# Kernel optimization log

Hardware: AMD Instinct MI355X
Metric: run time of the kernel (lower is better)

The kernel has to match this reference:

```python
import math
import jax, jax.numpy as jnp
import numpy as np

DIM = 1024
QK_DIM = 200
HIDDEN = 2 * DIM  # expansion_factor = 2
N = 8192


def setup_inputs() -> dict:
    key = jax.random.key(0)
    ks = jax.random.split(key, 8)
    s = 0.02
    return {
        "x": jax.random.normal(ks[0], (N, DIM), dtype=jnp.float32),
        "W_hidden": jax.random.normal(ks[1], (DIM, 2 * HIDDEN), dtype=jnp.float32) * s,
        "b_hidden": jnp.zeros((2 * HIDDEN,), dtype=jnp.float32),
        "W_qk": jax.random.normal(ks[2], (DIM, QK_DIM), dtype=jnp.float32) * s,
        "b_qk": jnp.zeros((QK_DIM,), dtype=jnp.float32),
        "gamma": 1.0 + jax.random.normal(ks[3], (2, QK_DIM), dtype=jnp.float32) * s,
        "beta": jnp.zeros((2, QK_DIM), dtype=jnp.float32),
        "W_out": jax.random.normal(ks[4], (HIDDEN, DIM), dtype=jnp.float32) * s,
        "b_out": jnp.zeros((DIM,), dtype=jnp.float32),
    }


def reference(x, W_hidden, b_hidden, W_qk, b_qk, gamma, beta, W_out, b_out):
    # to_hidden: Linear(dim -> 2*hidden) + SiLU, then chunk into v, gate
    hid = jax.nn.silu(x @ W_hidden + b_hidden)        # [N, 2H]
    v, gate = jnp.split(hid, 2, axis=-1)              # [N, H] each
    # to_qk: Linear(dim -> qk_dim) + SiLU
    qk = jax.nn.silu(x @ W_qk + b_qk)                 # [N, qk]
    # OffsetScale (heads=2): per-head affine on the shared qk
    q = qk * gamma[0] + beta[0]                       # [N, qk]
    k = qk * gamma[1] + beta[1]                       # [N, qk]
    # scores scaled by sqrt(dim) (module uses self.dim, not qk_dim)
    sim = (q @ k.T) * (1.0 / math.sqrt(x.shape[-1]))  # [N, N]
    # ReLU-squared attention (no softmax); dropout=0.0 -> identity
    attn = jnp.square(jax.nn.relu(sim))
    out = attn @ v                                    # [N, H]
    out = out * gate
    out = out @ W_out + b_out                         # [N, dim]
    # add_residual=True in this module multiplies by x
    return out * x
```

## Files before the change

### kernel.cpp

```cpp
#include <hip/hip_runtime.h>
#include <stdint.h>


typedef __bf16 bf16x8 __attribute__((ext_vector_type(8)));
typedef float f32x4 __attribute__((ext_vector_type(4)));

__device__ __forceinline__ uint16_t f2bf(float f) {
  uint32_t u = __builtin_bit_cast(uint32_t, f);
  u += 0x7fffu + ((u >> 16) & 1u);
  return (uint16_t)(u >> 16);
}
__device__ __forceinline__ float bf2f(uint16_t h) {
  uint32_t u = ((uint32_t)h) << 16;
  return __builtin_bit_cast(float, u);
}
__device__ __forceinline__ float silu_f(float s) {
  return s / (1.f + __expf(-s));
}

__device__ __forceinline__ void gload16(const void* g, void* l) {
  __builtin_amdgcn_global_load_lds(
      (__attribute__((address_space(1))) void*)const_cast<void*>(g),
      (__attribute__((address_space(3))) void*)l, 16, 0, 0);
}


__global__ void cast_to_bf16(const float* __restrict__ in, uint16_t* __restrict__ out, int n4) {
  int i = blockIdx.x * blockDim.x + threadIdx.x;
  if (i < n4) {
    float4 f = ((const float4*)in)[i];
    ushort4 o;
    o.x = f2bf(f.x); o.y = f2bf(f.y); o.z = f2bf(f.z); o.w = f2bf(f.w);
    ((ushort4*)out)[i] = o;
  }
}

__global__ void transpose_cast_pad(const float* __restrict__ in, uint16_t* __restrict__ out,
                                   int R, int C, int Cp) {
  __shared__ float tile[32][33];
  int cb = blockIdx.x * 32;
  int rb = blockIdx.y * 32;
  int tx = threadIdx.x;
  int ty = threadIdx.y;
#pragma unroll
  for (int i = 0; i < 4; ++i) {
    int r = rb + ty + i * 8;
    int c = cb + tx;
    tile[ty + i * 8][tx] = (c < C) ? in[(size_t)r * C + c] : 0.f;
  }
  __syncthreads();
#pragma unroll
  for (int i = 0; i < 4; ++i) {
    int c = cb + ty + i * 8;
    if (c < Cp) out[(size_t)c * R + rb + tx] = f2bf(tile[tx][ty + i * 8]);
  }
}


struct EpiParams {
  const float* bias;
  const float* bias2;
  const float* g0;
  const float* b0;
  const float* g1;
  const float* b1;
  const uint16_t* gate;
  const float* x;
  uint16_t* o16a;
  uint16_t* o16b;
  uint16_t* oq;
  uint16_t* ok;
  float* o32;
};

__global__ __launch_bounds__(256) void k_fused_hid_qk(
    const uint16_t* __restrict__ A, const uint16_t* __restrict__ Bt, EpiParams p) {
  __shared__ __align__(16) uint16_t As[128 * 32];
  __shared__ __align__(16) uint16_t Bs[128 * 32];

  const int tid = threadIdx.x;
  const int lane = tid & 63;
  const int wave = tid >> 6;
  const int wr = (wave >> 1) * 64;
  const int wc = (wave & 1) * 64;
  const int m0 = blockIdx.y * 128;
  const int n0 = blockIdx.x * 128;
  const int lda = 1024, ldb = 1024, K = 1024;

  f32x4 acc[4][4] = {};

  const int r0 = tid >> 2;
  const int q8 = (tid & 3) * 8;
  const uint16_t* gA0 = A + (size_t)(m0 + r0) * lda + q8;
  const uint16_t* gA1 = A + (size_t)(m0 + 64 + r0) * lda + q8;
  const uint16_t* gB0 = Bt + (size_t)(n0 + r0) * ldb + q8;
  const uint16_t* gB1 = Bt + (size_t)(n0 + 64 + r0) * ldb + q8;
  uint16_t* lA0 = As + wave * 512;
  uint16_t* lA1 = As + 2048 + wave * 512;
  uint16_t* lB0 = Bs + wave * 512;
  uint16_t* lB1 = Bs + 2048 + wave * 512;

  const int fr = lane & 15;
  const int kq = (lane >> 4) * 8;

  for (int k0 = 0; k0 < K; k0 += 32) {
    __syncthreads();
    gload16(gA0 + k0, lA0);
    gload16(gA1 + k0, lA1);
    gload16(gB0 + k0, lB0);
    gload16(gB1 + k0, lB1);
    __syncthreads();

    bf16x8 a[4], b[4];
#pragma unroll
    for (int i = 0; i < 4; ++i)
      a[i] = *(const bf16x8*)(As + (wr + i * 16 + fr) * 32 + kq);
#pragma unroll
    for (int j = 0; j < 4; ++j)
      b[j] = *(const bf16x8*)(Bs + (wc + j * 16 + fr) * 32 + kq);
#pragma unroll
    for (int i = 0; i < 4; ++i)
#pragma unroll
      for (int j = 0; j < 4; ++j)
        acc[i][j] = __builtin_amdgcn_mfma_f32_16x16x32_bf16(a[i], b[j], acc[i][j], 0, 0, 0);
  }

#pragma unroll
  for (int i = 0; i < 4; ++i) {
#pragma unroll
    for (int j = 0; j < 4; ++j) {
      const int row = m0 + wr + i * 16 + (lane >> 4) * 4;
      const int col = n0 + wc + j * 16 + fr;

      if (col < 2048) {
        const float bc = p.bias[col];
        ushort4 o;
        o.x = f2bf(silu_f(acc[i][j][0] + bc));
        o.y = f2bf(silu_f(acc[i][j][1] + bc));
        o.z = f2bf(silu_f(acc[i][j][2] + bc));
        o.w = f2bf(silu_f(acc[i][j][3] + bc));
        *(ushort4*)(p.o16a + (size_t)col * 8192 + row) = o;
      } else if (col < 4096) {
        const float bc = p.bias[col];
#pragma unroll
        for (int r = 0; r < 4; ++r)
          p.o16b[(size_t)(row + r) * 2048 + (col - 2048)] = f2bf(silu_f(acc[i][j][r] + bc));
      } else {
        const int qc = col - 4096;
        if (qc < 224) {
#pragma unroll
          for (int r = 0; r < 4; ++r) {
            float qv = 0.f, kv = 0.f;
            if (qc < 200) {
              float s = silu_f(acc[i][j][r] + p.bias2[qc]);
              qv = s * p.g0[qc] + p.b0[qc];
              kv = s * p.g1[qc] + p.b1[qc];
            }
            p.oq[(size_t)(row + r) * 224 + qc] = f2bf(qv);
            p.ok[(size_t)(row + r) * 224 + qc] = f2bf(kv);
          }
        }
      }
    }
  }
}

__global__ __launch_bounds__(256) void k_attn(
    const uint16_t* __restrict__ A,
    const uint16_t* __restrict__ Bt, EpiParams p) {
  __shared__ __align__(16) uint16_t As[128 * 32];
  __shared__ __align__(16) uint16_t Bs[128 * 32];
  __shared__ __align__(16) uint16_t Ep[4][2][16 * 72];

  const int tid = threadIdx.x;
  const int lane = tid & 63;
  const int wave = tid >> 6;
  const int wr = (wave >> 1) * 64;
  const int wc = (wave & 1) * 64;
  const int m0 = blockIdx.y * 128;
  const int n0 = blockIdx.x * 128;
  const int lda = 224, ldb = 224, K = 224;

  f32x4 acc[4][4] = {};

  const int r0 = tid >> 2;
  const int q8 = (tid & 3) * 8;
  const uint16_t* gA0 = A + (size_t)(m0 + r0) * lda + q8;
  const uint16_t* gA1 = A + (size_t)(m0 + 64 + r0) * lda + q8;
  const uint16_t* gB0 = Bt + (size_t)(n0 + r0) * ldb + q8;
  const uint16_t* gB1 = Bt + (size_t)(n0 + 64 + r0) * ldb + q8;
  uint16_t* lA0 = As + wave * 512;
  uint16_t* lA1 = As + 2048 + wave * 512;
  uint16_t* lB0 = Bs + wave * 512;
  uint16_t* lB1 = Bs + 2048 + wave * 512;

  const int fr = lane & 15;
  const int kq = (lane >> 4) * 8;

  for (int k0 = 0; k0 < K; k0 += 32) {
    __syncthreads();
    gload16(gA0 + k0, lA0);
    gload16(gA1 + k0, lA1);
    gload16(gB0 + k0, lB0);
    gload16(gB1 + k0, lB1);
    __syncthreads();

    bf16x8 a[4], b[4];
#pragma unroll
    for (int i = 0; i < 4; ++i)
      a[i] = *(const bf16x8*)(As + (wr + i * 16 + fr) * 32 + kq);
#pragma unroll
    for (int j = 0; j < 4; ++j)
      b[j] = *(const bf16x8*)(Bs + (wc + j * 16 + fr) * 32 + kq);
#pragma unroll
    for (int i = 0; i < 4; ++i)
#pragma unroll
      for (int j = 0; j < 4; ++j)
        acc[i][j] = __builtin_amdgcn_mfma_f32_16x16x32_bf16(a[i], b[j], acc[i][j], 0, 0, 0);
  }

#pragma unroll
  for (int i = 0; i < 4; ++i) {
    uint16_t* sl = Ep[wave][i & 1];
#pragma unroll
    for (int j = 0; j < 4; ++j) {
#pragma unroll
      for (int r = 0; r < 4; ++r) {
        float s = fmaxf(acc[i][j][r] * 0.03125f, 0.f);
        sl[((lane >> 4) * 4 + r) * 72 + j * 16 + fr] = f2bf(s * s);
      }
    }
    const int row = lane >> 2;
    const int c0 = (lane & 3) * 16;
    bf16x8 v0 = *(const bf16x8*)(sl + row * 72 + c0);
    bf16x8 v1 = *(const bf16x8*)(sl + row * 72 + c0 + 8);
    uint16_t* dst = p.o16a + (size_t)(m0 + wr + i * 16 + row) * 8192 + (n0 + wc + c0);
    *(bf16x8*)(dst) = v0;
    *(bf16x8*)(dst + 8) = v1;
  }
}

__global__ __launch_bounds__(512) void k_pv(
    const uint16_t* __restrict__ A, int lda,
    const uint16_t* __restrict__ Bt, int ldb,
    int K, int nx, EpiParams p) {
  __shared__ __align__(16) uint16_t As[128 * 32];
  __shared__ __align__(16) uint16_t Bs[256 * 32];

  const int id = blockIdx.x;
  const int bx = (id >> 3) % nx;
  const int by = (id & 7) + 8 * (id / (8 * nx));
  const int m0 = by * 128;
  const int n0 = bx * 256;

  const int tid = threadIdx.x;
  const int lane = tid & 63;
  const int wave = tid >> 6;
  const int wr = (wave & 1) * 64;
  const int wc = (wave >> 1) * 64;

  f32x4 acc[4][4] = {};

  const int r0 = tid >> 2;
  const int q8 = (tid & 3) * 8;
  const uint16_t* gA  = A  + (size_t)(m0 + r0) * lda + q8;
  const uint16_t* gB0 = Bt + (size_t)(n0 + r0) * ldb + q8;
  const uint16_t* gB1 = Bt + (size_t)(n0 + 128 + r0) * ldb + q8;
  uint16_t* lA  = As + wave * 512;
  uint16_t* lB0 = Bs + wave * 512;
  uint16_t* lB1 = Bs + 4096 + wave * 512;

  const int fr = lane & 15;
  const int kq = (lane >> 4) * 8;

  for (int k0 = 0; k0 < K; k0 += 32) {
    __syncthreads();
    gload16(gA + k0, lA);
    gload16(gB0 + k0, lB0);
    gload16(gB1 + k0, lB1);
    __syncthreads();

    bf16x8 a[4], b[4];
#pragma unroll
    for (int i = 0; i < 4; ++i)
      a[i] = *(const bf16x8*)(As + (wr + i * 16 + fr) * 32 + kq);
#pragma unroll
    for (int j = 0; j < 4; ++j)
      b[j] = *(const bf16x8*)(Bs + (wc + j * 16 + fr) * 32 + kq);
#pragma unroll
    for (int i = 0; i < 4; ++i)
#pragma unroll
      for (int j = 0; j < 4; ++j)
        acc[i][j] = __builtin_amdgcn_mfma_f32_16x16x32_bf16(a[i], b[j], acc[i][j], 0, 0, 0);
  }

#pragma unroll
  for (int i = 0; i < 4; ++i) {
#pragma unroll
    for (int j = 0; j < 4; ++j) {
      const int row = m0 + wr + i * 16 + (lane >> 4) * 4;
      const int col = n0 + wc + j * 16 + fr;
#pragma unroll
      for (int r = 0; r < 4; ++r) {
        float g = bf2f(p.gate[(size_t)(row + r) * 2048 + col]);
        p.o16a[(size_t)(row + r) * 2048 + col] = f2bf(acc[i][j][r] * g);
      }
    }
  }
}

__global__ __launch_bounds__(256) void k_final(
    const uint16_t* __restrict__ A,
    const uint16_t* __restrict__ Bt, EpiParams p) {
  __shared__ __align__(16) uint16_t As[128 * 32];
  __shared__ __align__(16) uint16_t Bs[128 * 32];

  const int tid = threadIdx.x;
  const int lane = tid & 63;
  const int wave = tid >> 6;
  const int wr = (wave >> 1) * 64;
  const int wc = (wave & 1) * 64;
  const int m0 = blockIdx.y * 128;
  const int n0 = blockIdx.x * 128;
  const int lda = 2048, ldb = 2048, K = 2048;

  f32x4 acc[4][4] = {};

  const int r0 = tid >> 2;
  const int q8 = (tid & 3) * 8;
  const uint16_t* gA0 = A + (size_t)(m0 + r0) * lda + q8;
  const uint16_t* gA1 = A + (size_t)(m0 + 64 + r0) * lda + q8;
  const uint16_t* gB0 = Bt + (size_t)(n0 + r0) * ldb + q8;
  const uint16_t* gB1 = Bt + (size_t)(n0 + 64 + r0) * ldb + q8;
  uint16_t* lA0 = As + wave * 512;
  uint16_t* lA1 = As + 2048 + wave * 512;
  uint16_t* lB0 = Bs + wave * 512;
  uint16_t* lB1 = Bs + 2048 + wave * 512;

  const int fr = lane & 15;
  const int kq = (lane >> 4) * 8;

  for (int k0 = 0; k0 < K; k0 += 32) {
    __syncthreads();
    gload16(gA0 + k0, lA0);
    gload16(gA1 + k0, lA1);
    gload16(gB0 + k0, lB0);
    gload16(gB1 + k0, lB1);
    __syncthreads();

    bf16x8 a[4], b[4];
#pragma unroll
    for (int i = 0; i < 4; ++i)
      a[i] = *(const bf16x8*)(As + (wr + i * 16 + fr) * 32 + kq);
#pragma unroll
    for (int j = 0; j < 4; ++j)
      b[j] = *(const bf16x8*)(Bs + (wc + j * 16 + fr) * 32 + kq);
#pragma unroll
    for (int i = 0; i < 4; ++i)
#pragma unroll
      for (int j = 0; j < 4; ++j)
        acc[i][j] = __builtin_amdgcn_mfma_f32_16x16x32_bf16(a[i], b[j], acc[i][j], 0, 0, 0);
  }

#pragma unroll
  for (int i = 0; i < 4; ++i) {
#pragma unroll
    for (int j = 0; j < 4; ++j) {
      const int row = m0 + wr + i * 16 + (lane >> 4) * 4;
      const int col = n0 + wc + j * 16 + fr;
      const float bc = p.bias[col];
#pragma unroll
      for (int r = 0; r < 4; ++r) {
        size_t idx = (size_t)(row + r) * 1024 + col;
        p.o32[idx] = (acc[i][j][r] + bc) * p.x[idx];
      }
    }
  }
}


extern "C" void kernel_launch(void* const* d_in, const int* in_sizes, int n_in,
                              void* d_out, int out_size, void* d_ws, size_t ws_size,
                              hipStream_t stream) {
  const float* x        = (const float*)d_in[0];
  const float* W_hidden = (const float*)d_in[1];
  const float* b_hidden = (const float*)d_in[2];
  const float* W_qk     = (const float*)d_in[3];
  const float* b_qk     = (const float*)d_in[4];
  const float* gamma    = (const float*)d_in[5];
  const float* beta     = (const float*)d_in[6];
  const float* W_out    = (const float*)d_in[7];
  const float* b_out    = (const float*)d_in[8];
  float* out = (float*)d_out;

  const bool fullM = ws_size >= (236ull << 20);
  const size_t region0 = fullM ? (128ull << 20) : (64ull << 20);

  char* base = (char*)d_ws;
  uint16_t* xb    = (uint16_t*)(base);
  uint16_t* WhT   = (uint16_t*)(base + (16ull << 20));
  uint16_t* WqkT  = (uint16_t*)(base + (24ull << 20));
  uint16_t* attnB = (uint16_t*)(base);
  char* tail = base + region0;
  uint16_t* WoT   = (uint16_t*)(tail);
  uint16_t* q     = (uint16_t*)(tail + (4ull << 20));
  uint16_t* kk    = (uint16_t*)(tail + (4ull << 20) + 3670016);
  uint16_t* vT    = (uint16_t*)(tail + (4ull << 20) + 2 * 3670016);
  uint16_t* gate  = (uint16_t*)(tail + (4ull << 20) + 2 * 3670016 + (32ull << 20));
  uint16_t* out2g = (uint16_t*)(tail + (4ull << 20) + 2 * 3670016 + (64ull << 20));
  (void)in_sizes; (void)n_in; (void)out_size;

  cast_to_bf16<<<(8192 * 1024 / 4) / 256, 256, 0, stream>>>(x, xb, 8192 * 1024 / 4);
  transpose_cast_pad<<<dim3(4096 / 32, 1024 / 32), dim3(32, 8), 0, stream>>>(W_hidden, WhT, 1024, 4096, 4096);
  transpose_cast_pad<<<dim3(256 / 32, 1024 / 32), dim3(32, 8), 0, stream>>>(W_qk, WqkT, 1024, 200, 256);
  transpose_cast_pad<<<dim3(1024 / 32, 2048 / 32), dim3(32, 8), 0, stream>>>(W_out, WoT, 2048, 1024, 1024);

  {
    EpiParams p{};
    p.bias = b_hidden; p.bias2 = b_qk;
    p.g0 = gamma; p.b0 = beta; p.g1 = gamma + 200; p.b1 = beta + 200;
    p.o16a = vT; p.o16b = gate; p.oq = q; p.ok = kk;
    k_fused_hid_qk<<<dim3(34, 64), 256, 0, stream>>>(xb, WhT, p);
  }

  if (fullM) {
    {
      EpiParams p{};
      p.o16a = attnB;
      k_attn<<<dim3(64, 64), 256, 0, stream>>>(q, kk, p);
    }
    {
      EpiParams p{};
      p.gate = gate; p.o16a = out2g;
      k_pv<<<dim3(8 * 64), 512, 0, stream>>>(attnB, 8192, vT, 8192, 8192, 8, p);
    }
  } else {
    for (int s = 0; s < 2; ++s) {
      {
        EpiParams p{};
        p.o16a = attnB;
        k_attn<<<dim3(64, 32), 256, 0, stream>>>(q + (size_t)s * 4096 * 224, kk, p);
      }
      {
        EpiParams p{};
        p.gate = gate + (size_t)s * 4096 * 2048;
        p.o16a = out2g + (size_t)s * 4096 * 2048;
        k_pv<<<dim3(8 * 32), 512, 0, stream>>>(attnB, 8192, vT, 8192, 8192, 8, p);
      }
    }
  }

  {
    EpiParams p{};
    p.bias = b_out; p.x = x; p.o32 = out;
    k_final<<<dim3(8, 64), 256, 0, stream>>>(out2g, WoT, p);
  }
}
```

Before: 668.1 us.

## Stage GEMM epilogues through LDS for coalesced stores; widen QK K-tile with swizzle

The hidden/QK GEMM epilogue now stages SiLU results through shared memory, so the transposed V and the gate are written as 16-byte coalesced rows instead of scattered 2-byte stores. The attention-score kernel pads q/k to 256 columns and loads 128-wide K tiles into XOR-swizzled LDS, which cuts the number of barriers and avoids bank conflicts. The PV epilogue also goes through LDS and applies the gate with vector loads. This trades more shared memory per block, and so possibly lower occupancy, and adds 56 columns of zero padding work to q@k.

```diff
diff --git a/kernel.cpp b/kernel.cpp
--- a/kernel.cpp
+++ b/kernel.cpp
@@ -9,10 +9,6 @@
   uint32_t u = __builtin_bit_cast(uint32_t, f);
   u += 0x7fffu + ((u >> 16) & 1u);
   return (uint16_t)(u >> 16);
-}
-__device__ __forceinline__ float bf2f(uint16_t h) {
-  uint32_t u = ((uint32_t)h) << 16;
-  return __builtin_bit_cast(float, u);
 }
 __device__ __forceinline__ float silu_f(float s) {
   return s / (1.f + __expf(-s));
@@ -73,10 +69,11 @@
   float* o32;
 };
 
-__global__ __launch_bounds__(256) void k_fused_hid_qk(
+__global__ __launch_bounds__(256) void k_hidqk(
     const uint16_t* __restrict__ A, const uint16_t* __restrict__ Bt, EpiParams p) {
-  __shared__ __align__(16) uint16_t As[128 * 32];
-  __shared__ __align__(16) uint16_t Bs[128 * 32];
+  __shared__ __align__(16) uint16_t SH[128 * 64];
+  uint16_t* As = SH;
+  uint16_t* Bs = SH + 4096;
 
   const int tid = threadIdx.x;
   const int lane = tid & 63;
@@ -101,7 +98,8 @@
   uint16_t* lB1 = Bs + 2048 + wave * 512;
 
   const int fr = lane & 15;
-  const int kq = (lane >> 4) * 8;
+  const int rg = lane >> 4;
+  const int kq = rg * 8;
 
   for (int k0 = 0; k0 < K; k0 += 32) {
     __syncthreads();
@@ -125,40 +123,63 @@
         acc[i][j] = __builtin_amdgcn_mfma_f32_16x16x32_bf16(a[i], b[j], acc[i][j], 0, 0, 0);
   }
 
-#pragma unroll
-  for (int i = 0; i < 4; ++i) {
+  if (n0 < 2048) {
+    __syncthreads();
+    uint16_t* ar = SH + wave * 2048;
+    const int lrow = lane >> 3;
+    const int mc = (lane & 7) * 8;
 #pragma unroll
     for (int j = 0; j < 4; ++j) {
-      const int row = m0 + wr + i * 16 + (lane >> 4) * 4;
-      const int col = n0 + wc + j * 16 + fr;
-
-      if (col < 2048) {
-        const float bc = p.bias[col];
-        ushort4 o;
-        o.x = f2bf(silu_f(acc[i][j][0] + bc));
-        o.y = f2bf(silu_f(acc[i][j][1] + bc));
-        o.z = f2bf(silu_f(acc[i][j][2] + bc));
-        o.w = f2bf(silu_f(acc[i][j][3] + bc));
-        *(ushort4*)(p.o16a + (size_t)col * 8192 + row) = o;
-      } else if (col < 4096) {
-        const float bc = p.bias[col];
+      const float bc = p.bias[n0 + wc + j * 16 + fr];
+#pragma unroll
+      for (int i = 0; i < 4; ++i)
 #pragma unroll
         for (int r = 0; r < 4; ++r)
-          p.o16b[(size_t)(row + r) * 2048 + (col - 2048)] = f2bf(silu_f(acc[i][j][r] + bc));
-      } else {
-        const int qc = col - 4096;
-        if (qc < 224) {
-#pragma unroll
-          for (int r = 0; r < 4; ++r) {
-            float qv = 0.f, kv = 0.f;
-            if (qc < 200) {
-              float s = silu_f(acc[i][j][r] + p.bias2[qc]);
-              qv = s * p.g0[qc] + p.b0[qc];
-              kv = s * p.g1[qc] + p.b1[qc];
-            }
-            p.oq[(size_t)(row + r) * 224 + qc] = f2bf(qv);
-            p.ok[(size_t)(row + r) * 224 + qc] = f2bf(kv);
+          ar[fr * 72 + i * 16 + rg * 4 + r] = f2bf(silu_f(acc[i][j][r] + bc));
+#pragma unroll
+      for (int rr = 0; rr < 2; ++rr) {
+        bf16x8 v = *(const bf16x8*)(ar + (rr * 8 + lrow) * 72 + mc);
+        *(bf16x8*)(p.o16a + (size_t)(n0 + wc + j * 16 + rr * 8 + lrow) * 8192 + m0 + wr + mc) = v;
+      }
+    }
+  } else if (n0 < 4096) {
+    __syncthreads();
+    uint16_t* ar = SH + wave * 2048;
+    const int lrow = lane >> 3;
+    const int nc = (lane & 7) * 8;
+    float bc[4];
+#pragma unroll
+    for (int j = 0; j < 4; ++j) bc[j] = p.bias[n0 + wc + j * 16 + fr];
+#pragma unroll
+    for (int i = 0; i < 4; ++i) {
+#pragma unroll
+      for (int j = 0; j < 4; ++j)
+#pragma unroll
+        for (int r = 0; r < 4; ++r)
+          ar[(rg * 4 + r) * 72 + j * 16 + fr] = f2bf(silu_f(acc[i][j][r] + bc[j]));
+#pragma unroll
+      for (int rr = 0; rr < 2; ++rr) {
+        bf16x8 v = *(const bf16x8*)(ar + (rr * 8 + lrow) * 72 + nc);
+        *(bf16x8*)(p.o16b + (size_t)(m0 + wr + i * 16 + rr * 8 + lrow) * 2048 + (n0 - 2048) + wc + nc) = v;
+      }
+    }
+  } else {
+#pragma unroll
+    for (int i = 0; i < 4; ++i) {
+#pragma unroll
+      for (int j = 0; j < 4; ++j) {
+        const int row = m0 + wr + i * 16 + rg * 4;
+        const int qc = n0 + wc + j * 16 + fr - 4096;
+#pragma unroll
+        for (int r = 0; r < 4; ++r) {
+          float qv = 0.f, kv = 0.f;
+          if (qc < 200) {
+            float s = silu_f(acc[i][j][r] + p.bias2[qc]);
+            qv = s * p.g0[qc] + p.b0[qc];
+            kv = s * p.g1[qc] + p.b1[qc];
           }
+          p.oq[(size_t)(row + r) * 256 + qc] = f2bf(qv);
+          p.ok[(size_t)(row + r) * 256 + qc] = f2bf(kv);
         }
       }
     }
@@ -166,11 +187,11 @@
 }
 
 __global__ __launch_bounds__(256) void k_attn(
-    const uint16_t* __restrict__ A,
-    const uint16_t* __restrict__ Bt, EpiParams p) {
-  __shared__ __align__(16) uint16_t As[128 * 32];
-  __shared__ __align__(16) uint16_t Bs[128 * 32];
-  __shared__ __align__(16) uint16_t Ep[4][2][16 * 72];
+    const uint16_t* __restrict__ Q,
+    const uint16_t* __restrict__ Kt,
+    uint16_t* __restrict__ attn) {
+  __shared__ __align__(16) uint16_t As[128 * 128];
+  __shared__ __align__(16) uint16_t Bs[128 * 128];
 
   const int tid = threadIdx.x;
   const int lane = tid & 63;
@@ -179,62 +200,57 @@
   const int wc = (wave & 1) * 64;
   const int m0 = blockIdx.y * 128;
   const int n0 = blockIdx.x * 128;
-  const int lda = 224, ldb = 224, K = 224;
+  const int fr = lane & 15;
+  const int rg = lane >> 4;
 
   f32x4 acc[4][4] = {};
 
-  const int r0 = tid >> 2;
-  const int q8 = (tid & 3) * 8;
-  const uint16_t* gA0 = A + (size_t)(m0 + r0) * lda + q8;
-  const uint16_t* gA1 = A + (size_t)(m0 + 64 + r0) * lda + q8;
-  const uint16_t* gB0 = Bt + (size_t)(n0 + r0) * ldb + q8;
-  const uint16_t* gB1 = Bt + (size_t)(n0 + 64 + r0) * ldb + q8;
-  uint16_t* lA0 = As + wave * 512;
-  uint16_t* lA1 = As + 2048 + wave * 512;
-  uint16_t* lB0 = Bs + wave * 512;
-  uint16_t* lB1 = Bs + 2048 + wave * 512;
-
-  const int fr = lane & 15;
-  const int kq = (lane >> 4) * 8;
-
-  for (int k0 = 0; k0 < K; k0 += 32) {
-    __syncthreads();
-    gload16(gA0 + k0, lA0);
-    gload16(gA1 + k0, lA1);
-    gload16(gB0 + k0, lB0);
-    gload16(gB1 + k0, lB1);
-    __syncthreads();
-
-    bf16x8 a[4], b[4];
-#pragma unroll
-    for (int i = 0; i < 4; ++i)
-      a[i] = *(const bf16x8*)(As + (wr + i * 16 + fr) * 32 + kq);
+  for (int ko = 0; ko < 256; ko += 128) {
+    __syncthreads();
+#pragma unroll
+    for (int t = 0; t < 8; ++t) {
+      const int s = t * 4 + wave;
+      const int row = s * 4 + rg;
+      const int log8 = fr ^ (row & 15);
+      gload16(Q + (size_t)(m0 + row) * 256 + ko + log8 * 8, As + s * 512);
+      gload16(Kt + (size_t)(n0 + row) * 256 + ko + log8 * 8, Bs + s * 512);
+    }
+    __syncthreads();
+
+#pragma unroll
+    for (int kc = 0; kc < 4; ++kc) {
+      bf16x8 a[4], b[4];
+#pragma unroll
+      for (int i = 0; i < 4; ++i)
+        a[i] = *(const bf16x8*)(As + (wr + i * 16 + fr) * 128 + (((kc * 4 + rg) ^ fr) * 8));
+#pragma unroll
+      for (int j = 0; j < 4; ++j)
+        b[j] = *(const bf16x8*)(Bs + (wc + j * 16 + fr) * 128 + (((kc * 4 + rg) ^ fr) * 8));
+#pragma unroll
+      for (int i = 0; i < 4; ++i)
+#pragma unroll
+        for (int j = 0; j < 4; ++j)
+          acc[i][j] = __builtin_amdgcn_mfma_f32_16x16x32_bf16(a[i], b[j], acc[i][j], 0, 0, 0);
+    }
+  }
+
+  __syncthreads();
+  uint16_t* sl0 = As + wave * 2304;
+#pragma unroll
+  for (int i = 0; i < 4; ++i) {
+    uint16_t* sl = sl0 + (i & 1) * 1152;
 #pragma unroll
     for (int j = 0; j < 4; ++j)
-      b[j] = *(const bf16x8*)(Bs + (wc + j * 16 + fr) * 32 + kq);
-#pragma unroll
-    for (int i = 0; i < 4; ++i)
-#pragma unroll
-      for (int j = 0; j < 4; ++j)
-        acc[i][j] = __builtin_amdgcn_mfma_f32_16x16x32_bf16(a[i], b[j], acc[i][j], 0, 0, 0);
-  }
-
-#pragma unroll
-  for (int i = 0; i < 4; ++i) {
-    uint16_t* sl = Ep[wave][i & 1];
-#pragma unroll
-    for (int j = 0; j < 4; ++j) {
 #pragma unroll
       for (int r = 0; r < 4; ++r) {
         float s = fmaxf(acc[i][j][r] * 0.03125f, 0.f);
-        sl[((lane >> 4) * 4 + r) * 72 + j * 16 + fr] = f2bf(s * s);
-      }
-    }
+        sl[(rg * 4 + r) * 72 + j * 16 + fr] = f2bf(s * s);
+      }
     const int row = lane >> 2;
     const int c0 = (lane & 3) * 16;
     bf16x8 v0 = *(const bf16x8*)(sl + row * 72 + c0);
     bf16x8 v1 = *(const bf16x8*)(sl + row * 72 + c0 + 8);
-    uint16_t* dst = p.o16a + (size_t)(m0 + wr + i * 16 + row) * 8192 + (n0 + wc + c0);
+    uint16_t* dst = attn + (size_t)(m0 + wr + i * 16 + row) * 8192 + (n0 + wc + c0);
     *(bf16x8*)(dst) = v0;
     *(bf16x8*)(dst + 8) = v1;
   }
@@ -244,8 +260,9 @@
     const uint16_t* __restrict__ A, int lda,
     const uint16_t* __restrict__ Bt, int ldb,
     int K, int nx, EpiParams p) {
-  __shared__ __align__(16) uint16_t As[128 * 32];
-  __shared__ __align__(16) uint16_t Bs[256 * 32];
+  __shared__ __align__(16) uint16_t SH[(128 + 256) * 32];
+  uint16_t* As = SH;
+  uint16_t* Bs = SH + 4096;
 
   const int id = blockIdx.x;
   const int bx = (id >> 3) % nx;
@@ -271,7 +288,8 @@
   uint16_t* lB1 = Bs + 4096 + wave * 512;
 
   const int fr = lane & 15;
-  const int kq = (lane >> 4) * 8;
+  const int rg = lane >> 4;
+  const int kq = rg * 8;
 
   for (int k0 = 0; k0 < K; k0 += 32) {
     __syncthreads();
@@ -294,17 +312,26 @@
         acc[i][j] = __builtin_amdgcn_mfma_f32_16x16x32_bf16(a[i], b[j], acc[i][j], 0, 0, 0);
   }
 
+  __syncthreads();
+  uint16_t* ar = SH + wave * 1536;
+  const int lrow = lane >> 3;
+  const int nc = (lane & 7) * 8;
 #pragma unroll
   for (int i = 0; i < 4; ++i) {
 #pragma unroll
-    for (int j = 0; j < 4; ++j) {
-      const int row = m0 + wr + i * 16 + (lane >> 4) * 4;
-      const int col = n0 + wc + j * 16 + fr;
-#pragma unroll
-      for (int r = 0; r < 4; ++r) {
-        float g = bf2f(p.gate[(size_t)(row + r) * 2048 + col]);
-        p.o16a[(size_t)(row + r) * 2048 + col] = f2bf(acc[i][j][r] * g);
-      }
+    for (int j = 0; j < 4; ++j)
+#pragma unroll
+      for (int r = 0; r < 4; ++r)
+        ar[(rg * 4 + r) * 72 + j * 16 + fr] = f2bf(acc[i][j][r]);
+#pragma unroll
+    for (int rr = 0; rr < 2; ++rr) {
+      const size_t base = (size_t)(m0 + wr + i * 16 + rr * 8 + lrow) * 2048 + n0 + wc + nc;
+      bf16x8 v = *(const bf16x8*)(ar + (rr * 8 + lrow) * 72 + nc);
+      bf16x8 g = *(const bf16x8*)(p.gate + base);
+      bf16x8 o;
+#pragma unroll
+      for (int e = 0; e < 8; ++e) o[e] = (__bf16)((float)v[e] * (float)g[e]);
+      *(bf16x8*)(p.o16a + base) = o;
     }
   }
 }
@@ -404,10 +431,10 @@
   char* tail = base + region0;
   uint16_t* WoT   = (uint16_t*)(tail);
   uint16_t* q     = (uint16_t*)(tail + (4ull << 20));
-  uint16_t* kk    = (uint16_t*)(tail + (4ull << 20) + 3670016);
-  uint16_t* vT    = (uint16_t*)(tail + (4ull << 20) + 2 * 3670016);
-  uint16_t* gate  = (uint16_t*)(tail + (4ull << 20) + 2 * 3670016 + (32ull << 20));
-  uint16_t* out2g = (uint16_t*)(tail + (4ull << 20) + 2 * 3670016 + (64ull << 20));
+  uint16_t* kk    = (uint16_t*)(tail + (8ull << 20));
+  uint16_t* vT    = (uint16_t*)(tail + (12ull << 20));
+  uint16_t* gate  = (uint16_t*)(tail + (44ull << 20));
+  uint16_t* out2g = (uint16_t*)(tail + (76ull << 20));
   (void)in_sizes; (void)n_in; (void)out_size;
 
   cast_to_bf16<<<(8192 * 1024 / 4) / 256, 256, 0, stream>>>(x, xb, 8192 * 1024 / 4);
@@ -420,15 +447,11 @@
     p.bias = b_hidden; p.bias2 = b_qk;
     p.g0 = gamma; p.b0 = beta; p.g1 = gamma + 200; p.b1 = beta + 200;
     p.o16a = vT; p.o16b = gate; p.oq = q; p.ok = kk;
-    k_fused_hid_qk<<<dim3(34, 64), 256, 0, stream>>>(xb, WhT, p);
+    k_hidqk<<<dim3(34, 64), 256, 0, stream>>>(xb, WhT, p);
   }
 
   if (fullM) {
-    {
-      EpiParams p{};
-      p.o16a = attnB;
-      k_attn<<<dim3(64, 64), 256, 0, stream>>>(q, kk, p);
-    }
+    k_attn<<<dim3(64, 64), 256, 0, stream>>>(q, kk, attnB);
     {
       EpiParams p{};
       p.gate = gate; p.o16a = out2g;
@@ -436,11 +459,7 @@
     }
   } else {
     for (int s = 0; s < 2; ++s) {
-      {
-        EpiParams p{};
-        p.o16a = attnB;
-        k_attn<<<dim3(64, 32), 256, 0, stream>>>(q + (size_t)s * 4096 * 224, kk, p);
-      }
+      k_attn<<<dim3(64, 32), 256, 0, stream>>>(q + (size_t)s * 4096 * 256, kk, attnB);
       {
         EpiParams p{};
         p.gate = gate + (size_t)s * 4096 * 2048;
```

New measurement: 698.1 us. +4.5%, slower.
